# Kernel tuning notes

Measured on AMD Instinct MI355X. Metric: run time of the kernel, lower is better.

The kernel has to match this reference:

```python
import jax, jax.numpy as jnp
import numpy as np

ALPHA = 0.5
EPS = 1e-10

def setup_inputs() -> dict:
    key = jax.random.key(0)
    k1, k2, k3, k4 = jax.random.split(key, 4)
    B, S, H = 8, 2048, 768
    query_embs = jax.random.normal(k1, (B, S, H), dtype=jnp.float32)
    key_embs = jax.random.normal(k2, (B, S, H), dtype=jnp.float32)
    q_mask = (jax.random.uniform(k3, (B, S)) > 0.1).astype(jnp.float32)
    k_mask = (jax.random.uniform(k4, (B, S)) > 0.1).astype(jnp.float32)
    q_mask = q_mask.at[:, 0].set(1.0)
    k_mask = k_mask.at[:, 0].set(1.0)
    return {"query_embs": query_embs, "key_embs": key_embs,
            "q_mask": q_mask, "k_mask": k_mask, "gumbel_temp": 1.0}

def _l2norm(x):
    # torch F.normalize: x / max(||x||, eps-ish); use rsqrt with tiny floor
    n = jnp.sqrt(jnp.sum(x * x, axis=-1, keepdims=True))
    return x / jnp.maximum(n, 1e-12)

def reference(query_embs, key_embs, q_mask, k_mask, gumbel_temp):
    B, S, H = query_embs.shape
    q = _l2norm(query_embs)
    k = _l2norm(key_embs)
    sim = jnp.einsum('bqh,bkh->bqk', q, k)  # [B,S,S]
    # exponential distance decay w_{ij} = exp(-alpha*|i-j|)
    pos = jnp.arange(S)
    dist = jnp.abs(pos[:, None] - pos[None, :]).astype(sim.dtype)
    sim = sim * jnp.exp(-ALPHA * dist)
    valid = q_mask[:, :, None] * k_mask[:, None, :]  # [B,S,S]
    # eval path: no Gumbel noise
    noisy = sim / gumbel_temp
    noisy = noisy * valid - (1.0 - valid) * 1e9
    p = jax.nn.softmax(noisy, axis=-1)
    agg = jnp.einsum('bqk,bkh->bqh', p, k)
    scores = jnp.sum(q * agg, axis=-1) * q_mask  # [B,S]
    denom = jnp.maximum(jnp.sum(q_mask, axis=-1), 1.0)
    return jnp.sum(scores, axis=-1) / denom  # [B]
```

## Files before the change

### kernel.cpp

```cpp
#include <hip/hip_runtime.h>
#include <math.h>

#define SB 8
#define SS 2048
#define SH 768
#define ALPHA 0.5f
#define TI 16
#define NCH 5
#define RSH 776


typedef __fp16 f16x8 __attribute__((ext_vector_type(8)));
typedef float f32x4 __attribute__((ext_vector_type(4)));

__device__ __forceinline__ float dot4(float4 a, float4 b) {
  return a.x*b.x + a.y*b.y + a.z*b.z + a.w*b.w;
}
__device__ __forceinline__ unsigned int pk2(float a, float b) {
  return __builtin_bit_cast(unsigned int, __builtin_amdgcn_cvt_pkrtz(a, b));
}

__global__ __launch_bounds__(256) void kprep_kernel(
    const float* __restrict__ K, const float* __restrict__ km,
    const float* __restrict__ qm,
    float* __restrict__ kw, float* __restrict__ ksum,
    float* __restrict__ Nk, float* __restrict__ qsum) {
  __shared__ float4 red[4][3][64];
  int b = blockIdx.y, jc = blockIdx.x, t = threadIdx.x;
  int w = t >> 6, lane = t & 63;
  int j0 = jc * 32;
  float4 acc0 = {0,0,0,0}, acc1 = {0,0,0,0}, acc2 = {0,0,0,0};
  for (int jj = 0; jj < 8; ++jj) {
    int j = j0 + 8 * w + jj;
    const float4* rp = (const float4*)(K + ((size_t)b * SS + j) * SH);
    float4 a = rp[lane], b4 = rp[lane + 64], c4 = rp[lane + 128];
    float ss = dot4(a, a) + dot4(b4, b4) + dot4(c4, c4);
    #pragma unroll
    for (int m = 1; m < 64; m <<= 1) ss += __shfl_xor(ss, m, 64);
    float kwj = km[b * SS + j] / fmaxf(sqrtf(ss), 1e-12f);
    if (lane == 0) kw[b * SS + j] = kwj;
    acc0.x += a.x*kwj;  acc0.y += a.y*kwj;  acc0.z += a.z*kwj;  acc0.w += a.w*kwj;
    acc1.x += b4.x*kwj; acc1.y += b4.y*kwj; acc1.z += b4.z*kwj; acc1.w += b4.w*kwj;
    acc2.x += c4.x*kwj; acc2.y += c4.y*kwj; acc2.z += c4.z*kwj; acc2.w += c4.w*kwj;
  }
  red[w][0][lane] = acc0; red[w][1][lane] = acc1; red[w][2][lane] = acc2;
  __syncthreads();
  if (t < 192) {
    int s = t >> 6, l = t & 63;
    float4 r0 = red[0][s][l], r1 = red[1][s][l], r2 = red[2][s][l], r3 = red[3][s][l];
    float* kp = ksum + b * SH + (s * 64 + l) * 4;
    atomicAdd(kp + 0, r0.x+r1.x+r2.x+r3.x);
    atomicAdd(kp + 1, r0.y+r1.y+r2.y+r3.y);
    atomicAdd(kp + 2, r0.z+r1.z+r2.z+r3.z);
    atomicAdd(kp + 3, r0.w+r1.w+r2.w+r3.w);
  }
  if (t < 32) {
    float pkm = km[b * SS + j0 + t];
    float pqm = qm[b * SS + j0 + t];
    #pragma unroll
    for (int m = 1; m < 32; m <<= 1) {
      pkm += __shfl_xor(pkm, m, 64);
      pqm += __shfl_xor(pqm, m, 64);
    }
    if (t == 0) { atomicAdd(&Nk[b], pkm); atomicAdd(&qsum[b], pqm); }
  }
}

__global__ __launch_bounds__(256, 4) void band_kernel(
    const float* __restrict__ Q, const float* __restrict__ K,
    const float* __restrict__ temp, const float* __restrict__ qm,
    const float* __restrict__ kw,
    const float* __restrict__ ksum, const float* __restrict__ Nkp,
    const float* __restrict__ qsum,
    float* __restrict__ acc, int* __restrict__ cnt, float* __restrict__ out) {
  __shared__ __fp16 kh[TI * RSH];
  __shared__ float sC[1024];
  __shared__ float tab_s[64];
  __shared__ float qws[TI], d0s[TI], kwc[TI];
  int tid = threadIdx.x;
  int w = tid >> 6, lane = tid & 63;
  int l15 = lane & 15, quad = lane >> 4;
  int blk = blockIdx.x;
  int work = (blk & 7) * 128 + (blk >> 3);
  int b = work >> 7;
  int i0 = (work & 127) * TI;
  if (tid < 64) {
    float invt = 1.0f / temp[0];
    tab_s[tid] = __expf(-ALPHA * fabsf((float)(tid - 31))) * invt;
  }
  f16x8 afr[6];
  {
    const float* qrow = Q + (size_t)(b * SS + i0 + l15) * SH + w * 192 + quad * 8;
    const float* ksb  = ksum + (size_t)b * SH + w * 192 + quad * 8;
    float ssp = 0.f, d0p = 0.f;
    #pragma unroll
    for (int s = 0; s < 6; ++s) {
      float4 x0 = *(const float4*)(qrow + 32 * s);
      float4 x1 = *(const float4*)(qrow + 32 * s + 4);
      float4 k0 = *(const float4*)(ksb + 32 * s);
      float4 k1 = *(const float4*)(ksb + 32 * s + 4);
      ssp += dot4(x0, x0) + dot4(x1, x1);
      d0p += dot4(x0, k0) + dot4(x1, k1);
      uint4 u = make_uint4(pk2(x0.x,x0.y), pk2(x0.z,x0.w),
                           pk2(x1.x,x1.y), pk2(x1.z,x1.w));
      afr[s] = __builtin_bit_cast(f16x8, u);
    }
    sC[(w * 64 + lane) * 2]     = ssp;
    sC[(w * 64 + lane) * 2 + 1] = d0p;
  }
  __syncthreads();
  if (tid < TI) {
    float ss = 0.f, dd = 0.f;
    #pragma unroll
    for (int p = 0; p < 16; ++p) {
      int idx = ((p >> 2) * 64 + (p & 3) * 16 + tid) * 2;
      ss += sC[idx]; dd += sC[idx + 1];
    }
    qws[tid] = qm[b * SS + i0 + tid] / fmaxf(sqrtf(ss), 1e-12f);
    d0s[tid] = dd;
  }
  float nk = Nkp[b];
  const float* Kb = K + (size_t)b * SS * SH;
  const float* kwb = kw + b * SS;

  int prow = tid >> 4, pseg = tid & 15;
  float4 pf[12];
  {
    int jcl = min(max(i0 - 32 + prow, 0), SS - 1);
    const float4* src = (const float4*)(Kb + (size_t)jcl * SH + pseg * 48);
    #pragma unroll
    for (int u = 0; u < 12; ++u) pf[u] = src[u];
  }

  float anv[4] = {0,0,0,0}, adv[4] = {0,0,0,0};
  for (int c = 0; c < NCH; ++c) {
    int jlo = i0 - 32 + 16 * c;
    __syncthreads();
    {
      uint4* dst = (uint4*)(kh + prow * RSH + pseg * 48);
      #pragma unroll
      for (int u = 0; u < 6; ++u) {
        float4 a = pf[2*u], bb = pf[2*u+1];
        dst[u] = make_uint4(pk2(a.x,a.y), pk2(a.z,a.w), pk2(bb.x,bb.y), pk2(bb.z,bb.w));
      }
      if (tid < TI) {
        int j = jlo + tid;
        kwc[tid] = (j >= 0 && j < SS) ? kwb[j] : 0.0f;
      }
    }
    __syncthreads();
    if (c + 1 < NCH) {
      int jcl = min(max(jlo + 16 + prow, 0), SS - 1);
      const float4* src = (const float4*)(Kb + (size_t)jcl * SH + pseg * 48);
      #pragma unroll
      for (int u = 0; u < 12; ++u) pf[u] = src[u];
    }
    f32x4 d = {0.f, 0.f, 0.f, 0.f};
    {
      const __fp16* bbase = kh + l15 * RSH + w * 192 + quad * 8;
      #pragma unroll
      for (int s = 0; s < 6; ++s) {
        f16x8 bf = *(const f16x8*)(bbase + 32 * s);
        d = __builtin_amdgcn_mfma_f32_16x16x32_f16(afr[s], bf, d, 0, 0, 0);
      }
    }
    {
      float4* cw = (float4*)sC;
      cw[w * 64 + lane] = make_float4(d[0], d[1], d[2], d[3]);
    }
    __syncthreads();
    if (w == 0) {
      const float4* cr = (const float4*)sC;
      float4 t0 = cr[lane], t1 = cr[64 + lane], t2 = cr[128 + lane], t3 = cr[192 + lane];
      float sx[4] = {t0.x+t1.x+t2.x+t3.x, t0.y+t1.y+t2.y+t3.y,
                     t0.z+t1.z+t2.z+t3.z, t0.w+t1.w+t2.w+t3.w};
      int base = jlo - i0 + 31 + l15;
      float kwv = kwc[l15];
      #pragma unroll
      for (int reg = 0; reg < 4; ++reg) {
        int rowl = quad * 4 + reg;
        float sv = sx[reg] * qws[rowl] * kwv;
        int idx = min(max(base - rowl, 0), 63);
        float ev = __expf(sv * tab_s[idx]) - 1.0f;
        anv[reg] += ev * sv;
        adv[reg] += ev;
      }
    }
  }

  if (w == 0) {
    float tot = 0.f;
    #pragma unroll
    for (int reg = 0; reg < 4; ++reg) {
      float an = anv[reg], ad = adv[reg];
      an += __shfl_xor(an, 1, 64); an += __shfl_xor(an, 2, 64);
      an += __shfl_xor(an, 4, 64); an += __shfl_xor(an, 8, 64);
      ad += __shfl_xor(ad, 1, 64); ad += __shfl_xor(ad, 2, 64);
      ad += __shfl_xor(ad, 4, 64); ad += __shfl_xor(ad, 8, 64);
      int rowl = quad * 4 + reg;
      tot += (qws[rowl] * d0s[rowl] + an) / (nk + ad);
    }
    tot += __shfl_xor(tot, 16, 64);
    tot += __shfl_xor(tot, 32, 64);
    if (lane == 0) {
      atomicAdd(&acc[b], tot);
      __threadfence();
      if (atomicAdd(&cnt[b], 1) == 127) {
        float a = atomicAdd(&acc[b], 0.0f);
        out[b] = a / fmaxf(qsum[b], 1.0f);
      }
    }
  }
}

extern "C" void kernel_launch(void* const* d_in, const int* in_sizes, int n_in,
                              void* d_out, int out_size, void* d_ws, size_t ws_size,
                              hipStream_t stream) {
  const float* Q    = (const float*)d_in[0];
  const float* K    = (const float*)d_in[1];
  const float* qm   = (const float*)d_in[2];
  const float* km   = (const float*)d_in[3];
  const float* temp = (const float*)d_in[4];
  float* ws   = (float*)d_ws;
  float* kw   = ws;
  float* ksum = ws + SB * SS;
  float* Nk   = ksum + SB * SH;
  float* qsum = Nk + 8;
  float* accb = qsum + 8;
  int*   cnt  = (int*)(accb + 8);
  float* outp = (float*)d_out;

  (void)hipMemsetAsync(ksum, 0, (SB * SH + 32) * sizeof(float), stream);

  kprep_kernel<<<dim3(64, SB), 256, 0, stream>>>(K, km, qm, kw, ksum, Nk, qsum);
  band_kernel<<<SB * (SS / TI), 256, 0, stream>>>(Q, K, temp, qm, kw, ksum, Nk,
                                                  qsum, accb, cnt, outp);
}
```

Baseline: 188.5 us.

## Prescale K to fp16 in prep and stream swizzled tiles via global_load_lds

Result: faster. 154.2 us (-18.2%).

```diff
diff --git a/kernel.cpp b/kernel.cpp
--- a/kernel.cpp
+++ b/kernel.cpp
@@ -5,22 +5,240 @@
 #define SS 2048
 #define SH 768
 #define ALPHA 0.5f
+
+typedef __fp16 f16x8 __attribute__((ext_vector_type(8)));
+typedef float f32x4 __attribute__((ext_vector_type(4)));
+
+__device__ __forceinline__ float dot4(float4 a, float4 b) {
+  return a.x*b.x + a.y*b.y + a.z*b.z + a.w*b.w;
+}
+__device__ __forceinline__ unsigned int pk2(float a, float b) {
+  return __builtin_bit_cast(unsigned int, __builtin_amdgcn_cvt_pkrtz(a, b));
+}
+__device__ __forceinline__ void gl_lds16(const void* g, void* l) {
+  __builtin_amdgcn_global_load_lds(
+      (__attribute__((address_space(1))) void*)g,
+      (__attribute__((address_space(3))) void*)l, 16, 0, 0);
+}
+
+
+#define TI4 64
+#define NCH4 4
+#define TILE_H (32 * SH)
+#define TILE_B (TILE_H * 2)
+
+__global__ __launch_bounds__(256) void kprep_kernel(
+    const float* __restrict__ K, const float* __restrict__ km,
+    const float* __restrict__ qm,
+    __fp16* __restrict__ Khs, float* __restrict__ ksum,
+    float* __restrict__ Nk, float* __restrict__ qsum) {
+  __shared__ float4 red[4][3][64];
+  int b = blockIdx.y, jc = blockIdx.x, t = threadIdx.x;
+  int w = t >> 6, lane = t & 63;
+  int j0 = jc * 32;
+  float4 acc0 = {0,0,0,0}, acc1 = {0,0,0,0}, acc2 = {0,0,0,0};
+  for (int jj = 0; jj < 8; ++jj) {
+    int j = j0 + 8 * w + jj;
+    const float4* rp = (const float4*)(K + ((size_t)b * SS + j) * SH);
+    float4 a = rp[lane], b4 = rp[lane + 64], c4 = rp[lane + 128];
+    float ssv = dot4(a, a) + dot4(b4, b4) + dot4(c4, c4);
+    #pragma unroll
+    for (int m = 1; m < 64; m <<= 1) ssv += __shfl_xor(ssv, m, 64);
+    float kwj = km[b * SS + j] / fmaxf(sqrtf(ssv), 1e-12f);
+    uint2* kr = (uint2*)(Khs + ((size_t)b * SS + j) * SH);
+    kr[lane]       = make_uint2(pk2(a.x*kwj,  a.y*kwj),  pk2(a.z*kwj,  a.w*kwj));
+    kr[lane + 64]  = make_uint2(pk2(b4.x*kwj, b4.y*kwj), pk2(b4.z*kwj, b4.w*kwj));
+    kr[lane + 128] = make_uint2(pk2(c4.x*kwj, c4.y*kwj), pk2(c4.z*kwj, c4.w*kwj));
+    acc0.x += a.x*kwj;  acc0.y += a.y*kwj;  acc0.z += a.z*kwj;  acc0.w += a.w*kwj;
+    acc1.x += b4.x*kwj; acc1.y += b4.y*kwj; acc1.z += b4.z*kwj; acc1.w += b4.w*kwj;
+    acc2.x += c4.x*kwj; acc2.y += c4.y*kwj; acc2.z += c4.z*kwj; acc2.w += c4.w*kwj;
+  }
+  red[w][0][lane] = acc0; red[w][1][lane] = acc1; red[w][2][lane] = acc2;
+  __syncthreads();
+  if (t < 192) {
+    int s = t >> 6, l = t & 63;
+    float4 r0 = red[0][s][l], r1 = red[1][s][l], r2 = red[2][s][l], r3 = red[3][s][l];
+    float* kp = ksum + b * SH + (s * 64 + l) * 4;
+    atomicAdd(kp + 0, r0.x+r1.x+r2.x+r3.x);
+    atomicAdd(kp + 1, r0.y+r1.y+r2.y+r3.y);
+    atomicAdd(kp + 2, r0.z+r1.z+r2.z+r3.z);
+    atomicAdd(kp + 3, r0.w+r1.w+r2.w+r3.w);
+  }
+  if (t < 32) {
+    float pkm = km[b * SS + j0 + t];
+    float pqm = qm[b * SS + j0 + t];
+    #pragma unroll
+    for (int m = 1; m < 32; m <<= 1) {
+      pkm += __shfl_xor(pkm, m, 64);
+      pqm += __shfl_xor(pqm, m, 64);
+    }
+    if (t == 0) { atomicAdd(&Nk[b], pkm); atomicAdd(&qsum[b], pqm); }
+  }
+}
+
+__global__ __launch_bounds__(256, 1) void band_kernel(
+    const float* __restrict__ Q, const __fp16* __restrict__ Khs,
+    const float* __restrict__ temp, const float* __restrict__ qm,
+    const float* __restrict__ ksum, const float* __restrict__ Nkp,
+    const float* __restrict__ qsum,
+    float* __restrict__ acc, int* __restrict__ cnt, float* __restrict__ out) {
+  __shared__ __fp16 kh[2 * TILE_H];
+  __shared__ float tab_s[64];
+  __shared__ float wred[4];
+  int tid = threadIdx.x;
+  int w = tid >> 6, lane = tid & 63;
+  int l15 = lane & 15, quad = lane >> 4;
+  int blk = blockIdx.x;
+  int work = (blk & 7) * 32 + (blk >> 3);
+  int b = work >> 5;
+  int i0 = (work & 31) * TI4;
+
+  if (tid < 64) {
+    float invt = 1.0f / temp[0];
+    tab_s[tid] = __expf(-ALPHA * fabsf((float)(tid - 31))) * invt;
+  }
+
+  int qrow = i0 + w * 16 + l15;
+  float qmv = qm[b * SS + qrow];
+  float nk = Nkp[b];
+
+  int srcoff[12];
+  {
+    int base = (w << 10) + (lane << 4);
+    #pragma unroll
+    for (int u = 0; u < 12; ++u) {
+      int d = base + (u << 12);
+      int r = d / 1536;
+      int cb = d - r * 1536;
+      srcoff[u] = r * 1536 + (cb ^ ((r & 7) << 4));
+    }
+  }
+
+  const float* qp = Q + ((size_t)b * SS + qrow) * SH + quad * 8;
+  const float* kp = ksum + (size_t)b * SH + quad * 8;
+  f16x8 afr[24];
+  float ss = 0.f, dd = 0.f;
+  #pragma unroll
+  for (int s = 0; s < 24; ++s) {
+    float4 x0 = *(const float4*)(qp + 32 * s);
+    float4 x1 = *(const float4*)(qp + 32 * s + 4);
+    float4 k0 = *(const float4*)(kp + 32 * s);
+    float4 k1 = *(const float4*)(kp + 32 * s + 4);
+    ss += dot4(x0, x0) + dot4(x1, x1);
+    dd += dot4(x0, k0) + dot4(x1, k1);
+    uint4 u = make_uint4(pk2(x0.x, x0.y), pk2(x0.z, x0.w),
+                         pk2(x1.x, x1.y), pk2(x1.z, x1.w));
+    afr[s] = __builtin_bit_cast(f16x8, u);
+  }
+
+  const __fp16* KbH = Khs + (size_t)b * SS * SH;
+  auto stage = [&](int c) {
+    int jlo = i0 - 32 + 32 * c;
+    int jcl = min(max(jlo, 0), SS - 32);
+    const char* src = (const char*)KbH + (size_t)jcl * (SH * 2);
+    char* dst = (char*)kh + (c & 1) * TILE_B + (w << 10);
+    #pragma unroll
+    for (int u = 0; u < 12; ++u)
+      gl_lds16(src + srcoff[u], dst + (u << 12));
+  };
+  stage(0);
+
+  ss += __shfl_xor(ss, 16, 64); ss += __shfl_xor(ss, 32, 64);
+  dd += __shfl_xor(dd, 16, 64); dd += __shfl_xor(dd, 32, 64);
+  float qw = qmv / fmaxf(sqrtf(ss), 1e-12f);
+  float qwsr[4], d0r[4];
+  #pragma unroll
+  for (int r = 0; r < 4; ++r) {
+    qwsr[r] = __shfl(qw, quad * 4 + r, 64);
+    d0r[r]  = __shfl(dd, quad * 4 + r, 64);
+  }
+
+  float an[2][4] = {{0,0,0,0},{0,0,0,0}};
+  float ad[2][4] = {{0,0,0,0},{0,0,0,0}};
+  asm volatile("s_waitcnt lgkmcnt(0)" ::: "memory");
+
+  for (int c = 0; c < NCH4; ++c) {
+    if (c + 1 < NCH4) {
+      stage(c + 1);
+      __builtin_amdgcn_sched_barrier(0);
+      asm volatile("s_waitcnt vmcnt(12)" ::: "memory");
+    } else {
+      asm volatile("s_waitcnt vmcnt(0)" ::: "memory");
+    }
+    __builtin_amdgcn_s_barrier();
+    __builtin_amdgcn_sched_barrier(0);
+
+    const __fp16* tb = kh + (c & 1) * TILE_H;
+    int ro0 = l15 * SH, ro1 = (l15 + 16) * SH;
+    int xr = (l15 & 7) << 3;
+    f32x4 d0a = {0,0,0,0}, d0b = {0,0,0,0}, d1a = {0,0,0,0}, d1b = {0,0,0,0};
+    #pragma unroll
+    for (int s = 0; s < 24; ++s) {
+      int cc = ((quad << 3) + (s << 5)) ^ xr;
+      f16x8 b0 = *(const f16x8*)(tb + ro0 + cc);
+      f16x8 b1 = *(const f16x8*)(tb + ro1 + cc);
+      if (s & 1) {
+        d0b = __builtin_amdgcn_mfma_f32_16x16x32_f16(afr[s], b0, d0b, 0, 0, 0);
+        d1b = __builtin_amdgcn_mfma_f32_16x16x32_f16(afr[s], b1, d1b, 0, 0, 0);
+      } else {
+        d0a = __builtin_amdgcn_mfma_f32_16x16x32_f16(afr[s], b0, d0a, 0, 0, 0);
+        d1a = __builtin_amdgcn_mfma_f32_16x16x32_f16(afr[s], b1, d1a, 0, 0, 0);
+      }
+    }
+    asm volatile("" ::: "memory");
+    __builtin_amdgcn_s_barrier();
+    asm volatile("" ::: "memory");
+
+    int jlo = i0 - 32 + 32 * c;
+    f32x4 dt0 = d0a + d0b, dt1 = d1a + d1b;
+    #pragma unroll
+    for (int tk = 0; tk < 2; ++tk) {
+      f32x4 dt = tk ? dt1 : dt0;
+      int j = jlo + tk * 16 + l15;
+      float vmask = ((unsigned)j < SS) ? 1.0f : 0.0f;
+      int idxbase = j - i0 - w * 16 + 31;
+      #pragma unroll
+      for (int reg = 0; reg < 4; ++reg) {
+        float sv = dt[reg] * qwsr[reg];
+        int idx = min(max(idxbase - quad * 4 - reg, 0), 63);
+        float ev = (__expf(sv * tab_s[idx]) - 1.0f) * vmask;
+        an[tk][reg] += ev * sv;
+        ad[tk][reg] += ev;
+      }
+    }
+  }
+
+  float tot = 0.f;
+  #pragma unroll
+  for (int reg = 0; reg < 4; ++reg) {
+    float a = an[0][reg] + an[1][reg];
+    float e = ad[0][reg] + ad[1][reg];
+    a += __shfl_xor(a, 1, 64); a += __shfl_xor(a, 2, 64);
+    a += __shfl_xor(a, 4, 64); a += __shfl_xor(a, 8, 64);
+    e += __shfl_xor(e, 1, 64); e += __shfl_xor(e, 2, 64);
+    e += __shfl_xor(e, 4, 64); e += __shfl_xor(e, 8, 64);
+    tot += (qwsr[reg] * d0r[reg] + a) / (nk + e);
+  }
+  tot += __shfl_xor(tot, 16, 64);
+  tot += __shfl_xor(tot, 32, 64);
+  if (lane == 0) wred[w] = tot;
+  __syncthreads();
+  if (tid == 0) {
+    float t = wred[0] + wred[1] + wred[2] + wred[3];
+    atomicAdd(&acc[b], t);
+    __threadfence();
+    if (atomicAdd(&cnt[b], 1) == (SS / TI4) - 1) {
+      float a2 = atomicAdd(&acc[b], 0.0f);
+      out[b] = a2 / fmaxf(qsum[b], 1.0f);
+    }
+  }
+}
+
 #define TI 16
 #define NCH 5
 #define RSH 776
 
-
-typedef __fp16 f16x8 __attribute__((ext_vector_type(8)));
-typedef float f32x4 __attribute__((ext_vector_type(4)));
-
-__device__ __forceinline__ float dot4(float4 a, float4 b) {
-  return a.x*b.x + a.y*b.y + a.z*b.z + a.w*b.w;
-}
-__device__ __forceinline__ unsigned int pk2(float a, float b) {
-  return __builtin_bit_cast(unsigned int, __builtin_amdgcn_cvt_pkrtz(a, b));
-}
-
-__global__ __launch_bounds__(256) void kprep_kernel(
+__global__ __launch_bounds__(256) void kprep0_kernel(
     const float* __restrict__ K, const float* __restrict__ km,
     const float* __restrict__ qm,
     float* __restrict__ kw, float* __restrict__ ksum,
@@ -34,10 +252,10 @@
     int j = j0 + 8 * w + jj;
     const float4* rp = (const float4*)(K + ((size_t)b * SS + j) * SH);
     float4 a = rp[lane], b4 = rp[lane + 64], c4 = rp[lane + 128];
-    float ss = dot4(a, a) + dot4(b4, b4) + dot4(c4, c4);
-    #pragma unroll
-    for (int m = 1; m < 64; m <<= 1) ss += __shfl_xor(ss, m, 64);
-    float kwj = km[b * SS + j] / fmaxf(sqrtf(ss), 1e-12f);
+    float ssv = dot4(a, a) + dot4(b4, b4) + dot4(c4, c4);
+    #pragma unroll
+    for (int m = 1; m < 64; m <<= 1) ssv += __shfl_xor(ssv, m, 64);
+    float kwj = km[b * SS + j] / fmaxf(sqrtf(ssv), 1e-12f);
     if (lane == 0) kw[b * SS + j] = kwj;
     acc0.x += a.x*kwj;  acc0.y += a.y*kwj;  acc0.z += a.z*kwj;  acc0.w += a.w*kwj;
     acc1.x += b4.x*kwj; acc1.y += b4.y*kwj; acc1.z += b4.z*kwj; acc1.w += b4.w*kwj;
@@ -66,7 +284,7 @@
   }
 }
 
-__global__ __launch_bounds__(256, 4) void band_kernel(
+__global__ __launch_bounds__(256, 4) void band0_kernel(
     const float* __restrict__ Q, const float* __restrict__ K,
     const float* __restrict__ temp, const float* __restrict__ qm,
     const float* __restrict__ kw,
@@ -110,14 +328,14 @@
   }
   __syncthreads();
   if (tid < TI) {
-    float ss = 0.f, dd = 0.f;
+    float ssl = 0.f, ddl = 0.f;
     #pragma unroll
     for (int p = 0; p < 16; ++p) {
       int idx = ((p >> 2) * 64 + (p & 3) * 16 + tid) * 2;
-      ss += sC[idx]; dd += sC[idx + 1];
-    }
-    qws[tid] = qm[b * SS + i0 + tid] / fmaxf(sqrtf(ss), 1e-12f);
-    d0s[tid] = dd;
+      ssl += sC[idx]; ddl += sC[idx + 1];
+    }
+    qws[tid] = qm[b * SS + i0 + tid] / fmaxf(sqrtf(ssl), 1e-12f);
+    d0s[tid] = ddl;
   }
   float nk = Nkp[b];
   const float* Kb = K + (size_t)b * SS * SH;
@@ -192,13 +410,13 @@
     float tot = 0.f;
     #pragma unroll
     for (int reg = 0; reg < 4; ++reg) {
-      float an = anv[reg], ad = adv[reg];
-      an += __shfl_xor(an, 1, 64); an += __shfl_xor(an, 2, 64);
-      an += __shfl_xor(an, 4, 64); an += __shfl_xor(an, 8, 64);
-      ad += __shfl_xor(ad, 1, 64); ad += __shfl_xor(ad, 2, 64);
-      ad += __shfl_xor(ad, 4, 64); ad += __shfl_xor(ad, 8, 64);
+      float a = anv[reg], e = adv[reg];
+      a += __shfl_xor(a, 1, 64); a += __shfl_xor(a, 2, 64);
+      a += __shfl_xor(a, 4, 64); a += __shfl_xor(a, 8, 64);
+      e += __shfl_xor(e, 1, 64); e += __shfl_xor(e, 2, 64);
+      e += __shfl_xor(e, 4, 64); e += __shfl_xor(e, 8, 64);
       int rowl = quad * 4 + reg;
-      tot += (qws[rowl] * d0s[rowl] + an) / (nk + ad);
+      tot += (qws[rowl] * d0s[rowl] + a) / (nk + e);
     }
     tot += __shfl_xor(tot, 16, 64);
     tot += __shfl_xor(tot, 32, 64);
@@ -221,18 +439,33 @@
   const float* qm   = (const float*)d_in[2];
   const float* km   = (const float*)d_in[3];
   const float* temp = (const float*)d_in[4];
-  float* ws   = (float*)d_ws;
-  float* kw   = ws;
-  float* ksum = ws + SB * SS;
-  float* Nk   = ksum + SB * SH;
-  float* qsum = Nk + 8;
-  float* accb = qsum + 8;
-  int*   cnt  = (int*)(accb + 8);
   float* outp = (float*)d_out;
 
-  (void)hipMemsetAsync(ksum, 0, (SB * SH + 32) * sizeof(float), stream);
-
-  kprep_kernel<<<dim3(64, SB), 256, 0, stream>>>(K, km, qm, kw, ksum, Nk, qsum);
-  band_kernel<<<SB * (SS / TI), 256, 0, stream>>>(Q, K, temp, qm, kw, ksum, Nk,
-                                                  qsum, accb, cnt, outp);
-}
+  const size_t KHS_BYTES = (size_t)SB * SS * SH * 2;
+  const size_t NEED = KHS_BYTES + (size_t)(SB * SH + 32) * sizeof(float);
+
+  if (ws_size >= NEED) {
+    __fp16* Khs = (__fp16*)d_ws;
+    float* ksum = (float*)((char*)d_ws + KHS_BYTES);
+    float* Nk   = ksum + SB * SH;
+    float* qsum = Nk + 8;
+    float* accb = qsum + 8;
+    int*   cnt  = (int*)(accb + 8);
+    (void)hipMemsetAsync(ksum, 0, (SB * SH + 32) * sizeof(float), stream);
+    kprep_kernel<<<dim3(64, SB), 256, 0, stream>>>(K, km, qm, Khs, ksum, Nk, qsum);
+    band_kernel<<<SB * (SS / TI4), 256, 0, stream>>>(Q, Khs, temp, qm, ksum, Nk,
+                                                     qsum, accb, cnt, outp);
+  } else {
+    float* ws   = (float*)d_ws;
+    float* kw   = ws;
+    float* ksum = ws + SB * SS;
+    float* Nk   = ksum + SB * SH;
+    float* qsum = Nk + 8;
+    float* accb = qsum + 8;
+    int*   cnt  = (int*)(accb + 8);
+    (void)hipMemsetAsync(ksum, 0, (SB * SH + 32) * sizeof(float), stream);
+    kprep0_kernel<<<dim3(64, SB), 256, 0, stream>>>(K, km, qm, kw, ksum, Nk, qsum);
+    band0_kernel<<<SB * (SS / TI), 256, 0, stream>>>(Q, K, temp, qm, kw, ksum, Nk,
+                                                     qsum, accb, cnt, outp);
+  }
+}
```

## Pre-normalize K to fp16 in prep and load band operands straight to registers

Applied to the files above, without the earlier changes.

Measured after the change: 179.2 us. 4.9% less time.

```diff
diff --git a/kernel.cpp b/kernel.cpp
--- a/kernel.cpp
+++ b/kernel.cpp
@@ -5,10 +5,6 @@
 #define SS 2048
 #define SH 768
 #define ALPHA 0.5f
-#define TI 16
-#define NCH 5
-#define RSH 776
-
 
 typedef __fp16 f16x8 __attribute__((ext_vector_type(8)));
 typedef float f32x4 __attribute__((ext_vector_type(4)));
@@ -19,11 +15,12 @@
 __device__ __forceinline__ unsigned int pk2(float a, float b) {
   return __builtin_bit_cast(unsigned int, __builtin_amdgcn_cvt_pkrtz(a, b));
 }
+
 
 __global__ __launch_bounds__(256) void kprep_kernel(
     const float* __restrict__ K, const float* __restrict__ km,
     const float* __restrict__ qm,
-    float* __restrict__ kw, float* __restrict__ ksum,
+    __fp16* __restrict__ Khs, float* __restrict__ ksum,
     float* __restrict__ Nk, float* __restrict__ qsum) {
   __shared__ float4 red[4][3][64];
   int b = blockIdx.y, jc = blockIdx.x, t = threadIdx.x;
@@ -34,11 +31,14 @@
     int j = j0 + 8 * w + jj;
     const float4* rp = (const float4*)(K + ((size_t)b * SS + j) * SH);
     float4 a = rp[lane], b4 = rp[lane + 64], c4 = rp[lane + 128];
-    float ss = dot4(a, a) + dot4(b4, b4) + dot4(c4, c4);
-    #pragma unroll
-    for (int m = 1; m < 64; m <<= 1) ss += __shfl_xor(ss, m, 64);
-    float kwj = km[b * SS + j] / fmaxf(sqrtf(ss), 1e-12f);
-    if (lane == 0) kw[b * SS + j] = kwj;
+    float ssv = dot4(a, a) + dot4(b4, b4) + dot4(c4, c4);
+    #pragma unroll
+    for (int m = 1; m < 64; m <<= 1) ssv += __shfl_xor(ssv, m, 64);
+    float kwj = km[b * SS + j] / fmaxf(sqrtf(ssv), 1e-12f);
+    uint2* kr = (uint2*)(Khs + ((size_t)b * SS + j) * SH);
+    kr[lane]       = make_uint2(pk2(a.x*kwj,  a.y*kwj),  pk2(a.z*kwj,  a.w*kwj));
+    kr[lane + 64]  = make_uint2(pk2(b4.x*kwj, b4.y*kwj), pk2(b4.z*kwj, b4.w*kwj));
+    kr[lane + 128] = make_uint2(pk2(c4.x*kwj, c4.y*kwj), pk2(c4.z*kwj, c4.w*kwj));
     acc0.x += a.x*kwj;  acc0.y += a.y*kwj;  acc0.z += a.z*kwj;  acc0.w += a.w*kwj;
     acc1.x += b4.x*kwj; acc1.y += b4.y*kwj; acc1.z += b4.z*kwj; acc1.w += b4.w*kwj;
     acc2.x += c4.x*kwj; acc2.y += c4.y*kwj; acc2.z += c4.z*kwj; acc2.w += c4.w*kwj;
@@ -66,149 +66,123 @@
   }
 }
 
-__global__ __launch_bounds__(256, 4) void band_kernel(
-    const float* __restrict__ Q, const float* __restrict__ K,
+__global__ __launch_bounds__(256, 1) void band_kernel(
+    const float* __restrict__ Q, const __fp16* __restrict__ Khs,
     const float* __restrict__ temp, const float* __restrict__ qm,
-    const float* __restrict__ kw,
     const float* __restrict__ ksum, const float* __restrict__ Nkp,
     const float* __restrict__ qsum,
     float* __restrict__ acc, int* __restrict__ cnt, float* __restrict__ out) {
-  __shared__ __fp16 kh[TI * RSH];
-  __shared__ float sC[1024];
   __shared__ float tab_s[64];
-  __shared__ float qws[TI], d0s[TI], kwc[TI];
   int tid = threadIdx.x;
   int w = tid >> 6, lane = tid & 63;
   int l15 = lane & 15, quad = lane >> 4;
   int blk = blockIdx.x;
-  int work = (blk & 7) * 128 + (blk >> 3);
-  int b = work >> 7;
-  int i0 = (work & 127) * TI;
-  if (tid < 64) {
+  int work = (blk & 7) * 32 + (blk >> 3);
+  int b = work >> 5;
+  int i0 = (work & 31) * 64;
+  int i0w = i0 + 16 * w;
+  int qrow = i0w + l15;
+
+  float qmv = qm[b * SS + qrow];
+  float nk = Nkp[b];
+  {
     float invt = 1.0f / temp[0];
-    tab_s[tid] = __expf(-ALPHA * fabsf((float)(tid - 31))) * invt;
-  }
-  f16x8 afr[6];
+    tab_s[lane] = __expf(-ALPHA * fabsf((float)(lane - 31))) * invt;
+  }
+  asm volatile("s_waitcnt lgkmcnt(0)" ::: "memory");
+
+  const float* qp = Q + ((size_t)b * SS + qrow) * SH + quad * 8;
+  const float* kp = ksum + (size_t)b * SH + quad * 8;
+  f16x8 afr[24];
+  float ss = 0.f, dd = 0.f;
+  #pragma unroll
+  for (int s = 0; s < 24; ++s) {
+    float4 x0 = *(const float4*)(qp + 32 * s);
+    float4 x1 = *(const float4*)(qp + 32 * s + 4);
+    float4 k0 = *(const float4*)(kp + 32 * s);
+    float4 k1 = *(const float4*)(kp + 32 * s + 4);
+    ss += dot4(x0, x0) + dot4(x1, x1);
+    dd += dot4(x0, k0) + dot4(x1, k1);
+    uint4 u = make_uint4(pk2(x0.x, x0.y), pk2(x0.z, x0.w),
+                         pk2(x1.x, x1.y), pk2(x1.z, x1.w));
+    afr[s] = __builtin_bit_cast(f16x8, u);
+  }
+  ss += __shfl_xor(ss, 16, 64); ss += __shfl_xor(ss, 32, 64);
+  dd += __shfl_xor(dd, 16, 64); dd += __shfl_xor(dd, 32, 64);
+  float qw = qmv / fmaxf(sqrtf(ss), 1e-12f);
+  float qwsr[4], d0r[4];
+  #pragma unroll
+  for (int r = 0; r < 4; ++r) {
+    qwsr[r] = __shfl(qw, quad * 4 + r, 64);
+    d0r[r]  = __shfl(dd, quad * 4 + r, 64);
+  }
+
+  const __fp16* KbH = Khs + (size_t)b * SS * SH;
+  f16x8 bqA[12], bqB[12];
   {
-    const float* qrow = Q + (size_t)(b * SS + i0 + l15) * SH + w * 192 + quad * 8;
-    const float* ksb  = ksum + (size_t)b * SH + w * 192 + quad * 8;
-    float ssp = 0.f, d0p = 0.f;
-    #pragma unroll
-    for (int s = 0; s < 6; ++s) {
-      float4 x0 = *(const float4*)(qrow + 32 * s);
-      float4 x1 = *(const float4*)(qrow + 32 * s + 4);
-      float4 k0 = *(const float4*)(ksb + 32 * s);
-      float4 k1 = *(const float4*)(ksb + 32 * s + 4);
-      ssp += dot4(x0, x0) + dot4(x1, x1);
-      d0p += dot4(x0, k0) + dot4(x1, k1);
-      uint4 u = make_uint4(pk2(x0.x,x0.y), pk2(x0.z,x0.w),
-                           pk2(x1.x,x1.y), pk2(x1.z,x1.w));
-      afr[s] = __builtin_bit_cast(f16x8, u);
-    }
-    sC[(w * 64 + lane) * 2]     = ssp;
-    sC[(w * 64 + lane) * 2 + 1] = d0p;
-  }
-  __syncthreads();
-  if (tid < TI) {
-    float ss = 0.f, dd = 0.f;
-    #pragma unroll
-    for (int p = 0; p < 16; ++p) {
-      int idx = ((p >> 2) * 64 + (p & 3) * 16 + tid) * 2;
-      ss += sC[idx]; dd += sC[idx + 1];
-    }
-    qws[tid] = qm[b * SS + i0 + tid] / fmaxf(sqrtf(ss), 1e-12f);
-    d0s[tid] = dd;
-  }
-  float nk = Nkp[b];
-  const float* Kb = K + (size_t)b * SS * SH;
-  const float* kwb = kw + b * SS;
-
-  int prow = tid >> 4, pseg = tid & 15;
-  float4 pf[12];
-  {
-    int jcl = min(max(i0 - 32 + prow, 0), SS - 1);
-    const float4* src = (const float4*)(Kb + (size_t)jcl * SH + pseg * 48);
-    #pragma unroll
-    for (int u = 0; u < 12; ++u) pf[u] = src[u];
-  }
-
-  float anv[4] = {0,0,0,0}, adv[4] = {0,0,0,0};
-  for (int c = 0; c < NCH; ++c) {
-    int jlo = i0 - 32 + 16 * c;
-    __syncthreads();
-    {
-      uint4* dst = (uint4*)(kh + prow * RSH + pseg * 48);
+    int j = i0w - 32 + l15;
+    int jc = min(max(j, 0), SS - 1);
+    const __fp16* rp = KbH + (size_t)jc * SH + quad * 8;
+    #pragma unroll
+    for (int u = 0; u < 12; ++u) bqA[u] = *(const f16x8*)(rp + u * 32);
+  }
+  float an[4] = {0,0,0,0}, ad[4] = {0,0,0,0};
+  f32x4 da = {0,0,0,0}, db = {0,0,0,0};
+  #pragma unroll
+  for (int fi = 0; fi < 10; ++fi) {
+    const int t = fi >> 1, g = fi & 1;
+    if (fi < 9) {
+      const int tn = (fi + 1) >> 1, gn = (fi + 1) & 1;
+      int j = i0w - 32 + 16 * tn + l15;
+      int jc = min(max(j, 0), SS - 1);
+      const __fp16* rp = KbH + (size_t)jc * SH + gn * 384 + quad * 8;
       #pragma unroll
-      for (int u = 0; u < 6; ++u) {
-        float4 a = pf[2*u], bb = pf[2*u+1];
-        dst[u] = make_uint4(pk2(a.x,a.y), pk2(a.z,a.w), pk2(bb.x,bb.y), pk2(bb.z,bb.w));
+      for (int u = 0; u < 12; ++u) {
+        f16x8 v = *(const f16x8*)(rp + u * 32);
+        if (fi & 1) bqA[u] = v; else bqB[u] = v;
       }
-      if (tid < TI) {
-        int j = jlo + tid;
-        kwc[tid] = (j >= 0 && j < SS) ? kwb[j] : 0.0f;
-      }
-    }
-    __syncthreads();
-    if (c + 1 < NCH) {
-      int jcl = min(max(jlo + 16 + prow, 0), SS - 1);
-      const float4* src = (const float4*)(Kb + (size_t)jcl * SH + pseg * 48);
-      #pragma unroll
-      for (int u = 0; u < 12; ++u) pf[u] = src[u];
-    }
-    f32x4 d = {0.f, 0.f, 0.f, 0.f};
-    {
-      const __fp16* bbase = kh + l15 * RSH + w * 192 + quad * 8;
-      #pragma unroll
-      for (int s = 0; s < 6; ++s) {
-        f16x8 bf = *(const f16x8*)(bbase + 32 * s);
-        d = __builtin_amdgcn_mfma_f32_16x16x32_f16(afr[s], bf, d, 0, 0, 0);
-      }
-    }
-    {
-      float4* cw = (float4*)sC;
-      cw[w * 64 + lane] = make_float4(d[0], d[1], d[2], d[3]);
-    }
-    __syncthreads();
-    if (w == 0) {
-      const float4* cr = (const float4*)sC;
-      float4 t0 = cr[lane], t1 = cr[64 + lane], t2 = cr[128 + lane], t3 = cr[192 + lane];
-      float sx[4] = {t0.x+t1.x+t2.x+t3.x, t0.y+t1.y+t2.y+t3.y,
-                     t0.z+t1.z+t2.z+t3.z, t0.w+t1.w+t2.w+t3.w};
-      int base = jlo - i0 + 31 + l15;
-      float kwv = kwc[l15];
+    }
+    #pragma unroll
+    for (int u = 0; u < 12; ++u) {
+      f16x8 bv = (fi & 1) ? bqB[u] : bqA[u];
+      if (u & 1) db = __builtin_amdgcn_mfma_f32_16x16x32_f16(afr[g*12+u], bv, db, 0, 0, 0);
+      else       da = __builtin_amdgcn_mfma_f32_16x16x32_f16(afr[g*12+u], bv, da, 0, 0, 0);
+    }
+    if (g) {
+      f32x4 ds = da + db;
+      int j = i0w - 32 + 16 * t + l15;
+      float vmask = ((unsigned)j < SS) ? 1.0f : 0.0f;
+      int idxb = j - i0w + 31;
       #pragma unroll
       for (int reg = 0; reg < 4; ++reg) {
-        int rowl = quad * 4 + reg;
-        float sv = sx[reg] * qws[rowl] * kwv;
-        int idx = min(max(base - rowl, 0), 63);
-        float ev = __expf(sv * tab_s[idx]) - 1.0f;
-        anv[reg] += ev * sv;
-        adv[reg] += ev;
+        float sv = ds[reg] * qwsr[reg];
+        int idx = min(max(idxb - quad * 4 - reg, 0), 63);
+        float ev = (__expf(sv * tab_s[idx]) - 1.0f) * vmask;
+        an[reg] += ev * sv;
+        ad[reg] += ev;
       }
-    }
-  }
-
-  if (w == 0) {
-    float tot = 0.f;
-    #pragma unroll
-    for (int reg = 0; reg < 4; ++reg) {
-      float an = anv[reg], ad = adv[reg];
-      an += __shfl_xor(an, 1, 64); an += __shfl_xor(an, 2, 64);
-      an += __shfl_xor(an, 4, 64); an += __shfl_xor(an, 8, 64);
-      ad += __shfl_xor(ad, 1, 64); ad += __shfl_xor(ad, 2, 64);
-      ad += __shfl_xor(ad, 4, 64); ad += __shfl_xor(ad, 8, 64);
-      int rowl = quad * 4 + reg;
-      tot += (qws[rowl] * d0s[rowl] + an) / (nk + ad);
-    }
-    tot += __shfl_xor(tot, 16, 64);
-    tot += __shfl_xor(tot, 32, 64);
-    if (lane == 0) {
-      atomicAdd(&acc[b], tot);
-      __threadfence();
-      if (atomicAdd(&cnt[b], 1) == 127) {
-        float a = atomicAdd(&acc[b], 0.0f);
-        out[b] = a / fmaxf(qsum[b], 1.0f);
-      }
+      da = (f32x4){0,0,0,0}; db = (f32x4){0,0,0,0};
+    }
+  }
+
+  float tot = 0.f;
+  #pragma unroll
+  for (int reg = 0; reg < 4; ++reg) {
+    float a = an[reg], e = ad[reg];
+    a += __shfl_xor(a, 1, 64); a += __shfl_xor(a, 2, 64);
+    a += __shfl_xor(a, 4, 64); a += __shfl_xor(a, 8, 64);
+    e += __shfl_xor(e, 1, 64); e += __shfl_xor(e, 2, 64);
+    e += __shfl_xor(e, 4, 64); e += __shfl_xor(e, 8, 64);
+    tot += (qwsr[reg] * d0r[reg] + a) / (nk + e);
+  }
+  tot += __shfl_xor(tot, 16, 64);
+  tot += __shfl_xor(tot, 32, 64);
+  if (lane == 0) {
+    atomicAdd(&acc[b], tot);
+    __threadfence();
+    if (atomicAdd(&cnt[b], 1) == 127) {
+      float a2 = atomicAdd(&acc[b], 0.0f);
+      out[b] = a2 / fmaxf(qsum[b], 1.0f);
     }
   }
 }
@@ -221,18 +195,19 @@
   const float* qm   = (const float*)d_in[2];
   const float* km   = (const float*)d_in[3];
   const float* temp = (const float*)d_in[4];
-  float* ws   = (float*)d_ws;
-  float* kw   = ws;
-  float* ksum = ws + SB * SS;
+  float* outp = (float*)d_out;
+
+  const size_t KHS_BYTES = (size_t)SB * SS * SH * 2;
+  __fp16* Khs = (__fp16*)d_ws;
+  float* ksum = (float*)((char*)d_ws + KHS_BYTES);
   float* Nk   = ksum + SB * SH;
   float* qsum = Nk + 8;
   float* accb = qsum + 8;
   int*   cnt  = (int*)(accb + 8);
-  float* outp = (float*)d_out;
 
   (void)hipMemsetAsync(ksum, 0, (SB * SH + 32) * sizeof(float), stream);
 
-  kprep_kernel<<<dim3(64, SB), 256, 0, stream>>>(K, km, qm, kw, ksum, Nk, qsum);
-  band_kernel<<<SB * (SS / TI), 256, 0, stream>>>(Q, K, temp, qm, kw, ksum, Nk,
+  kprep_kernel<<<dim3(64, SB), 256, 0, stream>>>(K, km, qm, Khs, ksum, Nk, qsum);
+  band_kernel<<<SB * (SS / 64), 256, 0, stream>>>(Q, Khs, temp, qm, ksum, Nk,
                                                   qsum, accb, cnt, outp);
 }
```
